# Kernel tuning notes

Hardware: AMD Instinct MI355X
Metric: run time of the kernel (lower is better)

Reference implementation:

```python
import jax, jax.numpy as jnp
import numpy as np


def setup_inputs() -> dict:
    key = jax.random.key(0)
    k1, k2 = jax.random.split(key)
    inputs = jax.random.normal(k1, (16, 64, 64, 512), dtype=jnp.float32)
    gamma = jax.random.uniform(k2, (1,), dtype=jnp.float32)
    return {"inputs": inputs, "gamma": gamma}


def reference(inputs, gamma):
    # inputs: [B, H, W, C] -> vec_a: [B, HW, C]
    B, H, W, C = inputs.shape
    vec_a = inputs.reshape(B, H * W, C)
    # channel gram matrix: [B, C, C]
    aTa = jnp.einsum('bnc,bnd->bcd', vec_a, vec_a)
    # softmax over last axis (Keras Activation('softmax') default)
    attn = jax.nn.softmax(aTa, axis=-1)
    # attn @ a^T: [B, C, HW] -> transpose -> [B, HW, C]
    aaTa = jnp.einsum('bcd,bnd->bnc', attn, vec_a)
    out = gamma * aaTa.reshape(B, H, W, C) + inputs
    return out
```

## Files before the change

kernel.cpp:

```cpp
#include <hip/hip_runtime.h>

#define BATCH 16
#define NHW 4096
#define CH 512
#define SPLITK 2

typedef __attribute__((ext_vector_type(8))) short bf16x8;
typedef __attribute__((ext_vector_type(4))) short s16x4;
typedef __attribute__((ext_vector_type(4))) float f32x4;

__device__ __forceinline__ short f2bf(float f) {
  union { float f; unsigned u; } c; c.f = f;
  unsigned u = c.u;
  unsigned r = (u + 0x7FFFu + ((u >> 16) & 1u)) >> 16;
  return (short)r;
}

__device__ __forceinline__ void gload_lds16(const void* g, void* l) {
  __builtin_amdgcn_global_load_lds((const __attribute__((address_space(1))) unsigned*)g,
                                   (__attribute__((address_space(3))) unsigned*)l,
                                   16, 0, 0);
}

__device__ __forceinline__ void stage32(const short* __restrict__ g, int ld, int rowbase, int kk,
                                        short* lbase, int w, int l) {
#pragma unroll
  for (int i = 0; i < 4; ++i) {
    const int row = w * 32 + i * 8 + (l >> 3);
    const short* gs = g + (size_t)(rowbase + row) * ld + kk + (l & 7) * 8;
    short* ls = lbase + (w * 32 + i * 8) * 64;
    gload_lds16(gs, ls);
  }
}

__global__ __launch_bounds__(256) void cast_transpose(const float* __restrict__ in,
                                                      short* __restrict__ A16,
                                                      short* __restrict__ At16) {
  __shared__ short t[64][66];
  const int b = blockIdx.z;
  const int n0 = blockIdx.x * 64;
  const int c0 = blockIdx.y * 64;
  const int tid = threadIdx.x;
  const int rr = tid >> 4;
  const int cq = (tid & 15) * 4;
  const float* src = in + ((size_t)b * NHW + n0) * CH + c0;
  short* a = A16 + ((size_t)b * NHW + n0) * CH + c0;
#pragma unroll
  for (int i = 0; i < 4; ++i) {
    const int r = rr + i * 16;
    const float4 v = *(const float4*)(src + (size_t)r * CH + cq);
    s16x4 s;
    s.x = f2bf(v.x); s.y = f2bf(v.y); s.z = f2bf(v.z); s.w = f2bf(v.w);
    *(s16x4*)(a + (size_t)r * CH + cq) = s;
    t[cq + 0][r] = s.x; t[cq + 1][r] = s.y; t[cq + 2][r] = s.z; t[cq + 3][r] = s.w;
  }
  __syncthreads();
  short* at = At16 + ((size_t)b * CH + c0) * NHW + n0;
#pragma unroll
  for (int i = 0; i < 4; ++i) {
    const int c = rr + i * 16;
    s16x4 s;
    s.x = t[c][cq]; s.y = t[c][cq + 1]; s.z = t[c][cq + 2]; s.w = t[c][cq + 3];
    *(s16x4*)(at + (size_t)c * NHW + cq) = s;
  }
}

__global__ __launch_bounds__(256) void gram_kernel(const short* __restrict__ At,
                                                   float* __restrict__ Gp) {
  __shared__ short lds[32768];
  const int flat = blockIdx.x;
  const int wg = (flat & 7) * 64 + (flat >> 3);
  const int b = wg >> 5;
  const int r5 = wg & 31;
  const int kchunk = r5 >> 4;
  const int tile = r5 & 15;
  const int m0 = (tile >> 2) * 128;
  const int n0 = (tile & 3) * 128;
  const int kbase = kchunk * (NHW / SPLITK);

  const int tid = threadIdx.x;
  const int l = tid & 63;
  const int w = tid >> 6;
  const int wr = w >> 1, wc = w & 1;
  const short* Ab = At + (size_t)b * CH * NHW;

  f32x4 acc[4][4];
#pragma unroll
  for (int mi = 0; mi < 4; ++mi)
#pragma unroll
    for (int ni = 0; ni < 4; ++ni)
      acc[mi][ni] = (f32x4){0.f, 0.f, 0.f, 0.f};

  stage32(Ab, NHW, m0, kbase, lds, w, l);
  stage32(Ab, NHW, n0, kbase, lds + 8192, w, l);
  __syncthreads();

  const int nkt = (NHW / SPLITK) / 64;
  int cur = 0;
  for (int t = 0; t < nkt; ++t) {
    if (t + 1 < nkt) {
      short* nb = lds + (cur ^ 1) * 16384;
      stage32(Ab, NHW, m0, kbase + (t + 1) * 64, nb, w, l);
      stage32(Ab, NHW, n0, kbase + (t + 1) * 64, nb + 8192, w, l);
    }
    const short* As = lds + cur * 16384;
    const short* Bs = As + 8192;
#pragma unroll
    for (int ks = 0; ks < 2; ++ks) {
      const int ko = ks * 32 + (l >> 4) * 8;
      bf16x8 af[4], bfv[4];
#pragma unroll
      for (int mi = 0; mi < 4; ++mi)
        af[mi] = *(const bf16x8*)(As + (wr * 64 + mi * 16 + (l & 15)) * 64 + ko);
#pragma unroll
      for (int ni = 0; ni < 4; ++ni)
        bfv[ni] = *(const bf16x8*)(Bs + (wc * 64 + ni * 16 + (l & 15)) * 64 + ko);
#pragma unroll
      for (int mi = 0; mi < 4; ++mi)
#pragma unroll
        for (int ni = 0; ni < 4; ++ni)
          acc[mi][ni] = __builtin_amdgcn_mfma_f32_16x16x32_bf16(af[mi], bfv[ni], acc[mi][ni], 0, 0, 0);
    }
    __syncthreads();
    cur ^= 1;
  }

  float* G = Gp + (size_t)(kchunk * BATCH + b) * CH * CH;
#pragma unroll
  for (int mi = 0; mi < 4; ++mi)
#pragma unroll
    for (int ni = 0; ni < 4; ++ni) {
      const int col = n0 + wc * 64 + ni * 16 + (l & 15);
      const int rbase = m0 + wr * 64 + mi * 16 + (l >> 4) * 4;
#pragma unroll
      for (int j = 0; j < 4; ++j)
        G[(size_t)(rbase + j) * CH + col] = acc[mi][ni][j];
    }
}

__global__ __launch_bounds__(64) void softmax_kernel(const float* __restrict__ Gp,
                                                     short* __restrict__ P) {
  const int row = blockIdx.x;
  const int b = row >> 9;
  const int c = row & 511;
  const int l = threadIdx.x;
  const float* g0 = Gp + ((size_t)b * CH + c) * CH;
  const float* g1 = Gp + ((size_t)(BATCH + b) * CH + c) * CH;
  float v[8];
#pragma unroll
  for (int i = 0; i < 8; ++i) v[i] = g0[l + i * 64] + g1[l + i * 64];
  float m = v[0];
#pragma unroll
  for (int i = 1; i < 8; ++i) m = fmaxf(m, v[i]);
  for (int off = 32; off > 0; off >>= 1) m = fmaxf(m, __shfl_xor(m, off, 64));
  float s = 0.f;
#pragma unroll
  for (int i = 0; i < 8; ++i) { v[i] = __expf(v[i] - m); s += v[i]; }
  for (int off = 32; off > 0; off >>= 1) s += __shfl_xor(s, off, 64);
  const float inv = 1.0f / s;
  short* p = P + ((size_t)b * CH + c) * CH;
#pragma unroll
  for (int i = 0; i < 8; ++i) p[l + i * 64] = f2bf(v[i] * inv);
}

__global__ __launch_bounds__(256) void out_kernel(const short* __restrict__ A16,
                                                  const short* __restrict__ P,
                                                  const float* __restrict__ inp,
                                                  const float* __restrict__ gamma,
                                                  float* __restrict__ out) {
  __shared__ short lds[16384];
  const int flat = blockIdx.x;
  const int wg = (flat & 7) * 256 + (flat >> 3);
  const int b = wg >> 7;
  const int t7 = wg & 127;
  const int m0 = (t7 >> 2) * 128;
  const int n0 = (t7 & 3) * 128;

  const int tid = threadIdx.x;
  const int l = tid & 63;
  const int w = tid >> 6;
  const int wr = w >> 1, wc = w & 1;
  const short* Ab = A16 + (size_t)b * NHW * CH;
  const short* Pb = P + (size_t)b * CH * CH;

  f32x4 acc[4][4];
#pragma unroll
  for (int mi = 0; mi < 4; ++mi)
#pragma unroll
    for (int ni = 0; ni < 4; ++ni)
      acc[mi][ni] = (f32x4){0.f, 0.f, 0.f, 0.f};

  stage32(Ab, CH, m0, 0, lds, w, l);
  __syncthreads();

  int cur = 0;
#pragma unroll 1
  for (int kt = 0; kt < CH / 64; ++kt) {
    if (kt + 1 < CH / 64)
      stage32(Ab, CH, m0, (kt + 1) * 64, lds + (cur ^ 1) * 8192, w, l);
    const short* As = lds + cur * 8192;
#pragma unroll
    for (int ks = 0; ks < 2; ++ks) {
      const int ko = kt * 64 + ks * 32 + (l >> 4) * 8;
      bf16x8 af[4], bfv[4];
#pragma unroll
      for (int ni = 0; ni < 4; ++ni)
        bfv[ni] = *(const bf16x8*)(Pb + (size_t)(n0 + wc * 64 + ni * 16 + (l & 15)) * CH + ko);
#pragma unroll
      for (int mi = 0; mi < 4; ++mi)
        af[mi] = *(const bf16x8*)(As + (wr * 64 + mi * 16 + (l & 15)) * 64 + ks * 32 + (l >> 4) * 8);
#pragma unroll
      for (int mi = 0; mi < 4; ++mi)
#pragma unroll
        for (int ni = 0; ni < 4; ++ni)
          acc[mi][ni] = __builtin_amdgcn_mfma_f32_16x16x32_bf16(af[mi], bfv[ni], acc[mi][ni], 0, 0, 0);
    }
    __syncthreads();
    cur ^= 1;
  }

  const float gm = gamma[0];
  const float* ib = inp + (size_t)b * NHW * CH;
  float* ob = out + (size_t)b * NHW * CH;
#pragma unroll
  for (int mi = 0; mi < 4; ++mi)
#pragma unroll
    for (int ni = 0; ni < 4; ++ni) {
      const int col = n0 + wc * 64 + ni * 16 + (l & 15);
      const int rbase = m0 + wr * 64 + mi * 16 + (l >> 4) * 4;
#pragma unroll
      for (int j = 0; j < 4; ++j) {
        const size_t idx = (size_t)(rbase + j) * CH + col;
        ob[idx] = gm * acc[mi][ni][j] + ib[idx];
      }
    }
}

extern "C" void kernel_launch(void* const* d_in, const int* in_sizes, int n_in,
                              void* d_out, int out_size, void* d_ws, size_t ws_size,
                              hipStream_t stream) {
  const float* inp = (const float*)d_in[0];
  const float* gamma = (const float*)d_in[1];
  float* out = (float*)d_out;
  char* ws = (char*)d_ws;
  short* A16 = (short*)ws;
  short* At16 = (short*)(ws + (size_t)67108864);
  float* Gp = (float*)(ws + (size_t)134217728);
  short* P = (short*)(ws + (size_t)167772160);

  hipLaunchKernelGGL(cast_transpose, dim3(NHW / 64, CH / 64, BATCH), dim3(256), 0, stream,
                     inp, A16, At16);
  hipLaunchKernelGGL(gram_kernel, dim3(16 * SPLITK * BATCH), dim3(256), 0, stream, At16, Gp);
  hipLaunchKernelGGL(softmax_kernel, dim3(BATCH * CH), dim3(64), 0, stream, Gp, P);
  hipLaunchKernelGGL(out_kernel, dim3((NHW / 128) * (CH / 128) * BATCH), dim3(256), 0, stream,
                     A16, P, inp, gamma, out);
}
```

Measured before the change: 394.8 us.

## Stage P tiles in LDS, read residual from bf16 copy, simplify grid mapping

The output GEMM now stages both the activation and softmax-probability tiles into LDS with 32-wide K steps, replacing direct global loads of P fragments. The residual add reads the bf16 activation copy instead of the fp32 input, which cuts epilogue traffic but adds bf16 rounding error to the residual term. The block-index swizzles in the gram and output kernels are replaced by plain 3D grids, and the output kernel gets a launch-bounds occupancy hint. Halving the K step doubles the number of barriers per tile.

```diff
diff --git a/kernel.cpp b/kernel.cpp
--- a/kernel.cpp
+++ b/kernel.cpp
@@ -16,6 +16,12 @@
   return (short)r;
 }
 
+__device__ __forceinline__ float bf2f(short s) {
+  union { unsigned u; float f; } c;
+  c.u = ((unsigned)(unsigned short)s) << 16;
+  return c.f;
+}
+
 __device__ __forceinline__ void gload_lds16(const void* g, void* l) {
   __builtin_amdgcn_global_load_lds((const __attribute__((address_space(1))) unsigned*)g,
                                    (__attribute__((address_space(3))) unsigned*)l,
@@ -29,6 +35,17 @@
     const int row = w * 32 + i * 8 + (l >> 3);
     const short* gs = g + (size_t)(rowbase + row) * ld + kk + (l & 7) * 8;
     short* ls = lbase + (w * 32 + i * 8) * 64;
+    gload_lds16(gs, ls);
+  }
+}
+
+__device__ __forceinline__ void stage128x32(const short* __restrict__ g, int ld, int rowbase,
+                                            int kk, short* lbase, int w, int l) {
+#pragma unroll
+  for (int i = 0; i < 2; ++i) {
+    const int row = w * 32 + i * 16 + (l >> 2);
+    const short* gs = g + (size_t)(rowbase + row) * ld + kk + (l & 3) * 8;
+    short* ls = lbase + (w * 32 + i * 16) * 32;
     gload_lds16(gs, ls);
   }
 }
@@ -68,14 +85,10 @@
 __global__ __launch_bounds__(256) void gram_kernel(const short* __restrict__ At,
                                                    float* __restrict__ Gp) {
   __shared__ short lds[32768];
-  const int flat = blockIdx.x;
-  const int wg = (flat & 7) * 64 + (flat >> 3);
-  const int b = wg >> 5;
-  const int r5 = wg & 31;
-  const int kchunk = r5 >> 4;
-  const int tile = r5 & 15;
-  const int m0 = (tile >> 2) * 128;
-  const int n0 = (tile & 3) * 128;
+  const int b = blockIdx.z;
+  const int m0 = (blockIdx.x >> 2) * 128;
+  const int n0 = (blockIdx.x & 3) * 128;
+  const int kchunk = blockIdx.y;
   const int kbase = kchunk * (NHW / SPLITK);
 
   const int tid = threadIdx.x;
@@ -163,16 +176,13 @@
   for (int i = 0; i < 8; ++i) p[l + i * 64] = f2bf(v[i] * inv);
 }
 
-__global__ __launch_bounds__(256) void out_kernel(const short* __restrict__ A16,
-                                                  const short* __restrict__ P,
-                                                  const float* __restrict__ inp,
-                                                  const float* __restrict__ gamma,
-                                                  float* __restrict__ out) {
+__global__ __launch_bounds__(256, 4) void out_kernel(const short* __restrict__ A16,
+                                                     const short* __restrict__ P,
+                                                     const float* __restrict__ gamma,
+                                                     float* __restrict__ out) {
   __shared__ short lds[16384];
-  const int flat = blockIdx.x;
-  const int wg = (flat & 7) * 256 + (flat >> 3);
-  const int b = wg >> 7;
-  const int t7 = wg & 127;
+  const int b = blockIdx.z;
+  const int t7 = blockIdx.x;
   const int m0 = (t7 >> 2) * 128;
   const int n0 = (t7 & 3) * 128;
 
@@ -190,37 +200,38 @@
     for (int ni = 0; ni < 4; ++ni)
       acc[mi][ni] = (f32x4){0.f, 0.f, 0.f, 0.f};
 
-  stage32(Ab, CH, m0, 0, lds, w, l);
+  stage128x32(Ab, CH, m0, 0, lds, w, l);
+  stage128x32(Pb, CH, n0, 0, lds + 4096, w, l);
   __syncthreads();
 
   int cur = 0;
 #pragma unroll 1
-  for (int kt = 0; kt < CH / 64; ++kt) {
-    if (kt + 1 < CH / 64)
-      stage32(Ab, CH, m0, (kt + 1) * 64, lds + (cur ^ 1) * 8192, w, l);
+  for (int kt = 0; kt < CH / 32; ++kt) {
+    if (kt + 1 < CH / 32) {
+      short* nb = lds + (cur ^ 1) * 8192;
+      stage128x32(Ab, CH, m0, (kt + 1) * 32, nb, w, l);
+      stage128x32(Pb, CH, n0, (kt + 1) * 32, nb + 4096, w, l);
+    }
     const short* As = lds + cur * 8192;
-#pragma unroll
-    for (int ks = 0; ks < 2; ++ks) {
-      const int ko = kt * 64 + ks * 32 + (l >> 4) * 8;
-      bf16x8 af[4], bfv[4];
+    const short* Bs = As + 4096;
+    const int ko = (l >> 4) * 8;
+    bf16x8 af[4], bfv[4];
+#pragma unroll
+    for (int mi = 0; mi < 4; ++mi)
+      af[mi] = *(const bf16x8*)(As + (wr * 64 + mi * 16 + (l & 15)) * 32 + ko);
+#pragma unroll
+    for (int ni = 0; ni < 4; ++ni)
+      bfv[ni] = *(const bf16x8*)(Bs + (wc * 64 + ni * 16 + (l & 15)) * 32 + ko);
+#pragma unroll
+    for (int mi = 0; mi < 4; ++mi)
 #pragma unroll
       for (int ni = 0; ni < 4; ++ni)
-        bfv[ni] = *(const bf16x8*)(Pb + (size_t)(n0 + wc * 64 + ni * 16 + (l & 15)) * CH + ko);
-#pragma unroll
-      for (int mi = 0; mi < 4; ++mi)
-        af[mi] = *(const bf16x8*)(As + (wr * 64 + mi * 16 + (l & 15)) * 64 + ks * 32 + (l >> 4) * 8);
-#pragma unroll
-      for (int mi = 0; mi < 4; ++mi)
-#pragma unroll
-        for (int ni = 0; ni < 4; ++ni)
-          acc[mi][ni] = __builtin_amdgcn_mfma_f32_16x16x32_bf16(af[mi], bfv[ni], acc[mi][ni], 0, 0, 0);
-    }
+        acc[mi][ni] = __builtin_amdgcn_mfma_f32_16x16x32_bf16(af[mi], bfv[ni], acc[mi][ni], 0, 0, 0);
     __syncthreads();
     cur ^= 1;
   }
 
   const float gm = gamma[0];
-  const float* ib = inp + (size_t)b * NHW * CH;
   float* ob = out + (size_t)b * NHW * CH;
 #pragma unroll
   for (int mi = 0; mi < 4; ++mi)
@@ -231,7 +242,7 @@
 #pragma unroll
       for (int j = 0; j < 4; ++j) {
         const size_t idx = (size_t)(rbase + j) * CH + col;
-        ob[idx] = gm * acc[mi][ni][j] + ib[idx];
+        ob[idx] = gm * acc[mi][ni][j] + bf2f(Ab[idx]);
       }
     }
 }
@@ -250,8 +261,8 @@
 
   hipLaunchKernelGGL(cast_transpose, dim3(NHW / 64, CH / 64, BATCH), dim3(256), 0, stream,
                      inp, A16, At16);
-  hipLaunchKernelGGL(gram_kernel, dim3(16 * SPLITK * BATCH), dim3(256), 0, stream, At16, Gp);
+  hipLaunchKernelGGL(gram_kernel, dim3(16, SPLITK, BATCH), dim3(256), 0, stream, At16, Gp);
   hipLaunchKernelGGL(softmax_kernel, dim3(BATCH * CH), dim3(64), 0, stream, Gp, P);
-  hipLaunchKernelGGL(out_kernel, dim3((NHW / 128) * (CH / 128) * BATCH), dim3(256), 0, stream,
-                     A16, P, inp, gamma, out);
-}
+  hipLaunchKernelGGL(out_kernel, dim3((NHW / 128) * (CH / 128), 1, BATCH), dim3(256), 0, stream,
+                     A16, P, gamma, out);
+}
```

After: 364.1 us. 7.8% less time.
